# Optimization experiments

Hardware: AMD Instinct MI355X
Metric: run time of the kernel (lower is better)

Reference implementation:

```python
import jax, jax.numpy as jnp
import numpy as np

B, N, F_IN, H, HID = 2, 1024, 128, 4, 32  # batch, nodes, in_feat, heads, hidden per head


def setup_inputs() -> dict:
    key = jax.random.key(0)
    k1, k2, k3, k4 = jax.random.split(key, 4)
    node_feat = jax.random.normal(k1, (B, N, F_IN), dtype=jnp.float32)
    adj_mtx = jax.random.randint(k2, (B, N, N), 0, 2, dtype=jnp.int32)  # 0/1 adjacency
    # xavier_normal init for params
    W = jax.random.normal(k3, (F_IN, H * HID), dtype=jnp.float32) * np.sqrt(2.0 / (F_IN + H * HID))
    Wa = jax.random.normal(k4, (H, HID), dtype=jnp.float32) * np.sqrt(2.0 / (H + HID))
    return {"node_feat": node_feat, "adj_mtx": adj_mtx, "W": W, "Wa": Wa}


def reference(node_feat, adj_mtx, W, Wa):
    b, n, _ = node_feat.shape
    h, hid = Wa.shape
    # projected features: (B, H, N, hid)
    x = (node_feat @ W).reshape(b, n, h, hid).transpose(0, 2, 1, 3)
    # GATv2 additive scores: leaky_relu(x_i + x_j) . Wa  -> (B, H, N, N)
    s = jax.nn.leaky_relu(x[:, :, :, None, :] + x[:, :, None, :, :], negative_slope=0.2)
    e = jnp.einsum('bhijk,hk->bhij', s, Wa)
    # mask non-edges, softmax over neighbors j
    e = jnp.where(adj_mtx[:, None, :, :] > 0, e, -jnp.inf)
    att = jax.nn.softmax(e, axis=-1)
    # aggregate values: (B, H, N, hid)
    xp = jnp.einsum('bhij,bhjd->bhid', att, x)
    # concat heads -> (B, N, H*hid)
    return xp.transpose(0, 2, 1, 3).reshape(b, n, h * hid)
```

## Files before the change

kernel.cpp:

```cpp
#include <hip/hip_runtime.h>
#include <math.h>

#define BB 2
#define NN 1024
#define HH 4
#define F_IN 128
#define HID 32
#define TJ 64
#define NT (NN/TJ)
#define NC 2
#define CT (NT/NC)

#define LOG2E 1.44269504f

typedef unsigned long long u64;
typedef _Float16 f16;
typedef _Float16 f16x8 __attribute__((ext_vector_type(8)));
typedef _Float16 f16x4 __attribute__((ext_vector_type(4)));
typedef float f32x4 __attribute__((ext_vector_type(4)));

#define WS_X    0
#define WS_D6   1048576
#define WS_XT   1081344
#define WS_P    1605632
#define WS_LS   18382848

__global__ __launch_bounds__(128) void gat_proj_kernel(const float* __restrict__ feat,
        const float* __restrict__ W, const float* __restrict__ Wa,
        float* __restrict__ xout, f16* __restrict__ xt, float* __restrict__ d6) {
    const int RPB = 4;
    int blk = blockIdx.x;
    int b  = blk / (NN / RPB);
    int n0 = (blk % (NN / RPB)) * RPB;
    int t  = threadIdx.x;

    __shared__ float fs[RPB][F_IN];
#pragma unroll
    for (int e = 0; e < RPB; ++e) {
        int idx = e * 128 + t;
        int r = idx >> 7, f = idx & 127;
        fs[r][f] = feat[((size_t)(b*NN + n0 + r))*F_IN + f];
    }
    __syncthreads();

    float acc[RPB];
#pragma unroll
    for (int r = 0; r < RPB; ++r) acc[r] = 0.f;
    for (int f = 0; f < F_IN; ++f) {
        float w = W[f*(HH*HID) + t];
#pragma unroll
        for (int r = 0; r < RPB; ++r) acc[r] = fmaf(fs[r][f], w, acc[r]);
    }

    int h = t >> 5, k = t & 31;
    int bh = b*HH + h;
#pragma unroll
    for (int r = 0; r < RPB; ++r)
        xout[((size_t)bh*NN + n0 + r)*HID + k] = acc[r];
    {
        f16x4 hv;
#pragma unroll
        for (int r = 0; r < RPB; ++r) hv[r] = (f16)acc[r];
        *(f16x4*)(xt + ((size_t)bh*HID + k)*NN + n0) = hv;
    }
    float w_t = Wa[t];
#pragma unroll
    for (int r = 0; r < RPB; ++r) {
        float p = acc[r] * w_t;
#pragma unroll
        for (int off = 16; off >= 1; off >>= 1) p += __shfl_xor(p, off, 32);
        if (k == 0) d6[(size_t)bh*NN + n0 + r] = 0.6f * LOG2E * p;
    }
}

__device__ __forceinline__ float sload(float v) {
    return __uint_as_float(__builtin_amdgcn_readfirstlane(__float_as_uint(v)));
}

__global__ __launch_bounds__(256) void gat_score_kernel(const float* __restrict__ x,
                                                        const float* __restrict__ d6,
                                                        const int* __restrict__ adj,
                                                        const float* __restrict__ Wa,
                                                        f16* __restrict__ P,
                                                        float* __restrict__ lsp) {
    const int tid = threadIdx.x;
    const int w = __builtin_amdgcn_readfirstlane(tid >> 6);
    const int l = tid & 63;
    const int blk = blockIdx.x;
    const int bh = blk & 7;
    const int rest = blk >> 3;
    const int jc = rest & (NC - 1);
    const int i0 = (rest >> 1) << 3;
    const int h = bh & (HH - 1), b = bh >> 2;
    const int iA = i0 + 2*w, iB = iA + 1;

    const float* xbh = x  + (size_t)bh * NN * HID;
    const float* dbh = d6 + (size_t)bh * NN;
    const int* adjA = adj + ((size_t)b*NN + iA) * NN;
    const int* adjB = adj + ((size_t)b*NN + iB) * NN;

    float xiA[HID], xiB[HID], wa4[HID];
    {
        const float4* xAv = (const float4*)(xbh + (size_t)iA*HID);
        const float4* xBv = (const float4*)(xbh + (size_t)iB*HID);
        const float4* wav = (const float4*)(Wa + h*HID);
#pragma unroll
        for (int q = 0; q < 8; ++q) {
            float4 a = xAv[q], bq = xBv[q], wv = wav[q];
            xiA[4*q+0] = sload(a.x);  xiA[4*q+1] = sload(a.y);
            xiA[4*q+2] = sload(a.z);  xiA[4*q+3] = sload(a.w);
            xiB[4*q+0] = sload(bq.x); xiB[4*q+1] = sload(bq.y);
            xiB[4*q+2] = sload(bq.z); xiB[4*q+3] = sload(bq.w);
            wa4[4*q+0] = sload((0.4f*LOG2E)*wv.x); wa4[4*q+1] = sload((0.4f*LOG2E)*wv.y);
            wa4[4*q+2] = sload((0.4f*LOG2E)*wv.z); wa4[4*q+3] = sload((0.4f*LOG2E)*wv.w);
        }
    }
    float ciA = sload(dbh[iA]) - 8.0f;
    float ciB = sload(dbh[iB]) - 8.0f;

    __shared__ float xs[2][TJ][36];

    float lsA = 0.f, lsB = 0.f;
    f16* prA = P + ((size_t)bh << 20) + (size_t)iA * NN;
    f16* prB = P + ((size_t)bh << 20) + (size_t)iB * NN;

    const int r0 = tid >> 3,         q0 = (tid & 7) << 2;
    const int r1 = (tid + 256) >> 3, q1 = ((tid + 256) & 7) << 2;
    const float4* gsrc = (const float4*)xbh;
    const int t0 = jc * CT;
    float4 pre0 = gsrc[t0*512 + tid];
    float4 pre1 = gsrc[t0*512 + tid + 256];

    for (int tt = 0; tt < CT; ++tt) {
        const int tg = t0 + tt;
        const int bc = tt & 1;
        *(float4*)&xs[bc][r0][q0] = pre0;
        *(float4*)&xs[bc][r1][q1] = pre1;
        __syncthreads();
        if (tt + 1 < CT) {
            pre0 = gsrc[(tg + 1)*512 + tid];
            pre1 = gsrc[(tg + 1)*512 + tid + 256];
        }

        const int j = tg*TJ + l;
        u64 wA = __ballot(adjA[j] > 0);
        u64 wB = __ballot(adjB[j] > 0);
        float dj = dbh[j];

        float4 xj4[8];
#pragma unroll
        for (int q = 0; q < 8; ++q) xj4[q] = *(const float4*)&xs[bc][l][4*q];

        float sA0 = 0.f, sA1 = 0.f, sA2 = 0.f, sA3 = 0.f;
        float sB0 = 0.f, sB1 = 0.f, sB2 = 0.f, sB3 = 0.f;
#pragma unroll
        for (int q = 0; q < 8; ++q) {
            float4 xv = xj4[q];
            float v;
            v = xiA[4*q+0] + xv.x; sA0 = fmaf(wa4[4*q+0], fabsf(v), sA0);
            v = xiA[4*q+1] + xv.y; sA1 = fmaf(wa4[4*q+1], fabsf(v), sA1);
            v = xiA[4*q+2] + xv.z; sA2 = fmaf(wa4[4*q+2], fabsf(v), sA2);
            v = xiA[4*q+3] + xv.w; sA3 = fmaf(wa4[4*q+3], fabsf(v), sA3);
            v = xiB[4*q+0] + xv.x; sB0 = fmaf(wa4[4*q+0], fabsf(v), sB0);
            v = xiB[4*q+1] + xv.y; sB1 = fmaf(wa4[4*q+1], fabsf(v), sB1);
            v = xiB[4*q+2] + xv.z; sB2 = fmaf(wa4[4*q+2], fabsf(v), sB2);
            v = xiB[4*q+3] + xv.w; sB3 = fmaf(wa4[4*q+3], fabsf(v), sB3);
        }
        float eA = (ciA + dj) + ((sA0 + sA1) + (sA2 + sA3));
        float eB = (ciB + dj) + ((sB0 + sB1) + (sB2 + sB3));
        float peA = exp2f(eA), peB = exp2f(eB);
        float pA, pB;
        asm("v_cndmask_b32 %0, 0, %1, %2" : "=v"(pA) : "v"(peA), "s"(wA));
        asm("v_cndmask_b32 %0, 0, %1, %2" : "=v"(pB) : "v"(peB), "s"(wB));
        lsA += pA;
        lsB += pB;
        prA[j] = (f16)pA;
        prB[j] = (f16)pB;
    }

#pragma unroll
    for (int off = 32; off >= 1; off >>= 1) {
        lsA += __shfl_xor(lsA, off, 64);
        lsB += __shfl_xor(lsB, off, 64);
    }
    if (l == 0) {
        lsp[(size_t)jc*(8*NN) + bh*NN + iA] = lsA;
        lsp[(size_t)jc*(8*NN) + bh*NN + iB] = lsB;
    }
}

__global__ __launch_bounds__(64) void gat_agg_kernel(const f16* __restrict__ P,
                                                     const f16* __restrict__ xt,
                                                     const float* __restrict__ lsp,
                                                     float* __restrict__ out) {
    const int l = threadIdx.x;
    const int blk = blockIdx.x;
    const int bh = blk & 7;
    const int it = blk >> 3;
    const int i0 = it << 4;
    const int b = bh >> 2, h = bh & 3;

    const f16* Pb  = P  + ((size_t)bh << 20);
    const f16* xtb = xt + (size_t)bh * HID * NN;

    f32x4 acc0 = {0.f, 0.f, 0.f, 0.f};
    f32x4 acc1 = {0.f, 0.f, 0.f, 0.f};
    const int lrow = l & 15, lslot = (l >> 4) << 3;

#pragma unroll
    for (int jt = 0; jt < 32; ++jt) {
        const int joff = jt*32 + lslot;
        f16x8 af = *(const f16x8*)(Pb  + (size_t)(i0 + lrow)*NN + joff);
        f16x8 b0 = *(const f16x8*)(xtb + (size_t)lrow*NN + joff);
        f16x8 b1 = *(const f16x8*)(xtb + (size_t)(16 + lrow)*NN + joff);
        acc0 = __builtin_amdgcn_mfma_f32_16x16x32_f16(af, b0, acc0, 0, 0, 0);
        acc1 = __builtin_amdgcn_mfma_f32_16x16x32_f16(af, b1, acc1, 0, 0, 0);
    }

#pragma unroll
    for (int r = 0; r < 4; ++r) {
        int row = i0 + ((l >> 4) << 2) + r;
        float ls = lsp[bh*NN + row] + lsp[8*NN + bh*NN + row];
        float inv = 1.0f / ls;
        float* orow = out + ((size_t)(b*NN + row))*(HH*HID) + h*HID;
        orow[lrow]      = acc0[r] * inv;
        orow[16 + lrow] = acc1[r] * inv;
    }
}

extern "C" void kernel_launch(void* const* d_in, const int* in_sizes, int n_in,
                              void* d_out, int out_size, void* d_ws, size_t ws_size,
                              hipStream_t stream) {
    const float* node_feat = (const float*)d_in[0];
    const int*   adj_mtx   = (const int*)d_in[1];
    const float* W         = (const float*)d_in[2];
    const float* Wa        = (const float*)d_in[3];
    float* out = (float*)d_out;

    char* ws = (char*)d_ws;
    float* x_ws  = (float*)(ws + WS_X);
    float* d6_ws = (float*)(ws + WS_D6);
    f16*   xt_ws = (f16*)(ws + WS_XT);
    f16*   P_ws  = (f16*)(ws + WS_P);
    float* ls_ws = (float*)(ws + WS_LS);

    hipLaunchKernelGGL(gat_proj_kernel, dim3(BB*NN/4), dim3(128), 0, stream,
                       node_feat, W, Wa, x_ws, xt_ws, d6_ws);
    hipLaunchKernelGGL(gat_score_kernel, dim3(BB*HH*NN/8 * NC), dim3(256), 0, stream,
                       x_ws, d6_ws, adj_mtx, Wa, P_ws, ls_ws);
    hipLaunchKernelGGL(gat_agg_kernel, dim3(8 * 64), dim3(64), 0, stream,
                       P_ws, xt_ws, ls_ws, out);
}
```

Measured before the change: 42.33 us.

## Compute GATv2 scores in packed fp16 with fdot2, four rows per wave

The projection now stores x in fp16 instead of fp32. The score kernel computes |xi+xj| with packed half adds and sign masking, and accumulates against Wa using fdot2. Each wave now handles four query rows instead of two, and the LDS staging of xj tiles with its barriers is dropped in favour of direct global loads. This halves the bytes read for x and the ALU ops per score, at the cost of fp16 rounding in the attention logits and no LDS reuse of xj across waves.

```diff
diff --git a/kernel.cpp b/kernel.cpp
--- a/kernel.cpp
+++ b/kernel.cpp
@@ -7,27 +7,40 @@
 #define F_IN 128
 #define HID 32
 #define TJ 64
-#define NT (NN/TJ)
+#define NT 16
 #define NC 2
 #define CT (NT/NC)
 
 #define LOG2E 1.44269504f
 
 typedef unsigned long long u64;
+typedef unsigned int u32;
 typedef _Float16 f16;
+typedef _Float16 h2   __attribute__((ext_vector_type(2)));
+typedef _Float16 f16x4 __attribute__((ext_vector_type(4)));
 typedef _Float16 f16x8 __attribute__((ext_vector_type(8)));
-typedef _Float16 f16x4 __attribute__((ext_vector_type(4)));
 typedef float f32x4 __attribute__((ext_vector_type(4)));
 
-#define WS_X    0
-#define WS_D6   1048576
-#define WS_XT   1081344
-#define WS_P    1605632
-#define WS_LS   18382848
+#define WS_XH  0
+#define WS_D6  524288
+#define WS_XT  557056
+#define WS_P   1081344
+#define WS_LS  17858560
+
+#if __has_builtin(__builtin_amdgcn_fdot2)
+#define FDOT2(a, b, c) __builtin_amdgcn_fdot2((a), (b), (c), false)
+#else
+static __device__ __forceinline__ float FDOT2(h2 a, h2 b, float c) {
+    return fmaf((float)a[0], (float)b[0], fmaf((float)a[1], (float)b[1], c));
+}
+#endif
+
+template <typename D, typename S>
+static __device__ __forceinline__ D bcast(S s) { return __builtin_bit_cast(D, s); }
 
 __global__ __launch_bounds__(128) void gat_proj_kernel(const float* __restrict__ feat,
         const float* __restrict__ W, const float* __restrict__ Wa,
-        float* __restrict__ xout, f16* __restrict__ xt, float* __restrict__ d6) {
+        f16* __restrict__ xh, f16* __restrict__ xt, float* __restrict__ d6) {
     const int RPB = 4;
     int blk = blockIdx.x;
     int b  = blk / (NN / RPB);
@@ -56,7 +69,7 @@
     int bh = b*HH + h;
 #pragma unroll
     for (int r = 0; r < RPB; ++r)
-        xout[((size_t)bh*NN + n0 + r)*HID + k] = acc[r];
+        xh[((size_t)bh*NN + n0 + r)*HID + k] = (f16)acc[r];
     {
         f16x4 hv;
 #pragma unroll
@@ -73,11 +86,9 @@
     }
 }
 
-__device__ __forceinline__ float sload(float v) {
-    return __uint_as_float(__builtin_amdgcn_readfirstlane(__float_as_uint(v)));
-}
-
-__global__ __launch_bounds__(256) void gat_score_kernel(const float* __restrict__ x,
+__device__ __forceinline__ u32 srfl(u32 v) { return __builtin_amdgcn_readfirstlane(v); }
+
+__global__ __launch_bounds__(256) void gat_score_kernel(const f16* __restrict__ xh,
                                                         const float* __restrict__ d6,
                                                         const int* __restrict__ adj,
                                                         const float* __restrict__ Wa,
@@ -90,102 +101,101 @@
     const int bh = blk & 7;
     const int rest = blk >> 3;
     const int jc = rest & (NC - 1);
-    const int i0 = (rest >> 1) << 3;
-    const int h = bh & (HH - 1), b = bh >> 2;
-    const int iA = i0 + 2*w, iB = iA + 1;
-
-    const float* xbh = x  + (size_t)bh * NN * HID;
-    const float* dbh = d6 + (size_t)bh * NN;
-    const int* adjA = adj + ((size_t)b*NN + iA) * NN;
-    const int* adjB = adj + ((size_t)b*NN + iB) * NN;
-
-    float xiA[HID], xiB[HID], wa4[HID];
+    const int i0 = (rest >> 1) << 4;
+    const int h = bh & 3, b = bh >> 2;
+    const int ib = i0 + 4*w;
+
+    const u32* xhu = (const u32*)(xh + (size_t)bh*NN*HID);
+    const float* dbh = d6 + (size_t)bh*NN;
+
+    u32 wa2[16];
     {
-        const float4* xAv = (const float4*)(xbh + (size_t)iA*HID);
-        const float4* xBv = (const float4*)(xbh + (size_t)iB*HID);
-        const float4* wav = (const float4*)(Wa + h*HID);
-#pragma unroll
-        for (int q = 0; q < 8; ++q) {
-            float4 a = xAv[q], bq = xBv[q], wv = wav[q];
-            xiA[4*q+0] = sload(a.x);  xiA[4*q+1] = sload(a.y);
-            xiA[4*q+2] = sload(a.z);  xiA[4*q+3] = sload(a.w);
-            xiB[4*q+0] = sload(bq.x); xiB[4*q+1] = sload(bq.y);
-            xiB[4*q+2] = sload(bq.z); xiB[4*q+3] = sload(bq.w);
-            wa4[4*q+0] = sload((0.4f*LOG2E)*wv.x); wa4[4*q+1] = sload((0.4f*LOG2E)*wv.y);
-            wa4[4*q+2] = sload((0.4f*LOG2E)*wv.z); wa4[4*q+3] = sload((0.4f*LOG2E)*wv.w);
+        const float* wap = Wa + h*HID;
+#pragma unroll
+        for (int q = 0; q < 16; ++q) {
+            h2 hw;
+            hw[0] = (f16)((0.4f*LOG2E) * wap[2*q]);
+            hw[1] = (f16)((0.4f*LOG2E) * wap[2*q+1]);
+            wa2[q] = srfl(bcast<u32>(hw));
         }
     }
-    float ciA = sload(dbh[iA]) - 8.0f;
-    float ciB = sload(dbh[iB]) - 8.0f;
-
-    __shared__ float xs[2][TJ][36];
-
-    float lsA = 0.f, lsB = 0.f;
-    f16* prA = P + ((size_t)bh << 20) + (size_t)iA * NN;
-    f16* prB = P + ((size_t)bh << 20) + (size_t)iB * NN;
-
-    const int r0 = tid >> 3,         q0 = (tid & 7) << 2;
-    const int r1 = (tid + 256) >> 3, q1 = ((tid + 256) & 7) << 2;
-    const float4* gsrc = (const float4*)xbh;
-    const int t0 = jc * CT;
-    float4 pre0 = gsrc[t0*512 + tid];
-    float4 pre1 = gsrc[t0*512 + tid + 256];
+    u32 xi2[4][16];
+    float ci[4];
+#pragma unroll
+    for (int r = 0; r < 4; ++r) {
+        const u32* xr = xhu + (size_t)(ib + r)*16;
+#pragma unroll
+        for (int q = 0; q < 16; ++q) xi2[r][q] = srfl(xr[q]);
+        ci[r] = __uint_as_float(srfl(__float_as_uint(dbh[ib + r]))) - 8.0f;
+    }
+
+    const int* adj0 = adj + ((size_t)b*NN + ib + 0)*NN;
+    const int* adj1 = adj + ((size_t)b*NN + ib + 1)*NN;
+    const int* adj2 = adj + ((size_t)b*NN + ib + 2)*NN;
+    const int* adj3 = adj + ((size_t)b*NN + ib + 3)*NN;
+    f16* pr0 = P + ((size_t)bh << 20) + (size_t)(ib + 0)*NN;
+    f16* pr1 = P + ((size_t)bh << 20) + (size_t)(ib + 1)*NN;
+    f16* pr2 = P + ((size_t)bh << 20) + (size_t)(ib + 2)*NN;
+    f16* pr3 = P + ((size_t)bh << 20) + (size_t)(ib + 3)*NN;
+
+    float ls0 = 0.f, ls1 = 0.f, ls2 = 0.f, ls3 = 0.f;
 
     for (int tt = 0; tt < CT; ++tt) {
-        const int tg = t0 + tt;
-        const int bc = tt & 1;
-        *(float4*)&xs[bc][r0][q0] = pre0;
-        *(float4*)&xs[bc][r1][q1] = pre1;
-        __syncthreads();
-        if (tt + 1 < CT) {
-            pre0 = gsrc[(tg + 1)*512 + tid];
-            pre1 = gsrc[(tg + 1)*512 + tid + 256];
+        const int j = (jc*CT + tt)*TJ + l;
+        u64 m0 = __ballot(adj0[j] > 0);
+        u64 m1 = __ballot(adj1[j] > 0);
+        u64 m2 = __ballot(adj2[j] > 0);
+        u64 m3 = __ballot(adj3[j] > 0);
+        float dj = dbh[j];
+
+        const u32* xjp = xhu + (size_t)j*16;
+        uint4 xa = *(const uint4*)(xjp);
+        uint4 xb = *(const uint4*)(xjp + 4);
+        uint4 xc = *(const uint4*)(xjp + 8);
+        uint4 xd = *(const uint4*)(xjp + 12);
+        u32 xj[16] = {xa.x, xa.y, xa.z, xa.w, xb.x, xb.y, xb.z, xb.w,
+                      xc.x, xc.y, xc.z, xc.w, xd.x, xd.y, xd.z, xd.w};
+
+        float s0 = 0.f, s1 = 0.f, s2 = 0.f, s3 = 0.f;
+#pragma unroll
+        for (int q = 0; q < 16; ++q) {
+            h2 xjh = bcast<h2>(xj[q]);
+            h2 wq  = bcast<h2>(wa2[q]);
+            h2 v; u32 a;
+            v = bcast<h2>(xi2[0][q]) + xjh; a = bcast<u32>(v) & 0x7fff7fffu;
+            s0 = FDOT2(bcast<h2>(a), wq, s0);
+            v = bcast<h2>(xi2[1][q]) + xjh; a = bcast<u32>(v) & 0x7fff7fffu;
+            s1 = FDOT2(bcast<h2>(a), wq, s1);
+            v = bcast<h2>(xi2[2][q]) + xjh; a = bcast<u32>(v) & 0x7fff7fffu;
+            s2 = FDOT2(bcast<h2>(a), wq, s2);
+            v = bcast<h2>(xi2[3][q]) + xjh; a = bcast<u32>(v) & 0x7fff7fffu;
+            s3 = FDOT2(bcast<h2>(a), wq, s3);
         }
-
-        const int j = tg*TJ + l;
-        u64 wA = __ballot(adjA[j] > 0);
-        u64 wB = __ballot(adjB[j] > 0);
-        float dj = dbh[j];
-
-        float4 xj4[8];
-#pragma unroll
-        for (int q = 0; q < 8; ++q) xj4[q] = *(const float4*)&xs[bc][l][4*q];
-
-        float sA0 = 0.f, sA1 = 0.f, sA2 = 0.f, sA3 = 0.f;
-        float sB0 = 0.f, sB1 = 0.f, sB2 = 0.f, sB3 = 0.f;
-#pragma unroll
-        for (int q = 0; q < 8; ++q) {
-            float4 xv = xj4[q];
-            float v;
-            v = xiA[4*q+0] + xv.x; sA0 = fmaf(wa4[4*q+0], fabsf(v), sA0);
-            v = xiA[4*q+1] + xv.y; sA1 = fmaf(wa4[4*q+1], fabsf(v), sA1);
-            v = xiA[4*q+2] + xv.z; sA2 = fmaf(wa4[4*q+2], fabsf(v), sA2);
-            v = xiA[4*q+3] + xv.w; sA3 = fmaf(wa4[4*q+3], fabsf(v), sA3);
-            v = xiB[4*q+0] + xv.x; sB0 = fmaf(wa4[4*q+0], fabsf(v), sB0);
-            v = xiB[4*q+1] + xv.y; sB1 = fmaf(wa4[4*q+1], fabsf(v), sB1);
-            v = xiB[4*q+2] + xv.z; sB2 = fmaf(wa4[4*q+2], fabsf(v), sB2);
-            v = xiB[4*q+3] + xv.w; sB3 = fmaf(wa4[4*q+3], fabsf(v), sB3);
-        }
-        float eA = (ciA + dj) + ((sA0 + sA1) + (sA2 + sA3));
-        float eB = (ciB + dj) + ((sB0 + sB1) + (sB2 + sB3));
-        float peA = exp2f(eA), peB = exp2f(eB);
-        float pA, pB;
-        asm("v_cndmask_b32 %0, 0, %1, %2" : "=v"(pA) : "v"(peA), "s"(wA));
-        asm("v_cndmask_b32 %0, 0, %1, %2" : "=v"(pB) : "v"(peB), "s"(wB));
-        lsA += pA;
-        lsB += pB;
-        prA[j] = (f16)pA;
-        prB[j] = (f16)pB;
+        float p0 = exp2f(ci[0] + dj + s0);
+        float p1 = exp2f(ci[1] + dj + s1);
+        float p2 = exp2f(ci[2] + dj + s2);
+        float p3 = exp2f(ci[3] + dj + s3);
+        asm("v_cndmask_b32 %0, 0, %1, %2" : "=v"(p0) : "v"(p0), "s"(m0));
+        asm("v_cndmask_b32 %0, 0, %1, %2" : "=v"(p1) : "v"(p1), "s"(m1));
+        asm("v_cndmask_b32 %0, 0, %1, %2" : "=v"(p2) : "v"(p2), "s"(m2));
+        asm("v_cndmask_b32 %0, 0, %1, %2" : "=v"(p3) : "v"(p3), "s"(m3));
+        ls0 += p0; ls1 += p1; ls2 += p2; ls3 += p3;
+        pr0[j] = (f16)p0;
+        pr1[j] = (f16)p1;
+        pr2[j] = (f16)p2;
+        pr3[j] = (f16)p3;
     }
 
 #pragma unroll
     for (int off = 32; off >= 1; off >>= 1) {
-        lsA += __shfl_xor(lsA, off, 64);
-        lsB += __shfl_xor(lsB, off, 64);
+        ls0 += __shfl_xor(ls0, off, 64);
+        ls1 += __shfl_xor(ls1, off, 64);
+        ls2 += __shfl_xor(ls2, off, 64);
+        ls3 += __shfl_xor(ls3, off, 64);
     }
     if (l == 0) {
-        lsp[(size_t)jc*(8*NN) + bh*NN + iA] = lsA;
-        lsp[(size_t)jc*(8*NN) + bh*NN + iB] = lsB;
+        float* lp = lsp + (size_t)jc*(8*NN) + bh*NN + ib;
+        lp[0] = ls0; lp[1] = ls1; lp[2] = ls2; lp[3] = ls3;
     }
 }
 
@@ -238,16 +248,16 @@
     float* out = (float*)d_out;
 
     char* ws = (char*)d_ws;
-    float* x_ws  = (float*)(ws + WS_X);
+    f16*   xh_ws = (f16*)(ws + WS_XH);
     float* d6_ws = (float*)(ws + WS_D6);
     f16*   xt_ws = (f16*)(ws + WS_XT);
     f16*   P_ws  = (f16*)(ws + WS_P);
     float* ls_ws = (float*)(ws + WS_LS);
 
     hipLaunchKernelGGL(gat_proj_kernel, dim3(BB*NN/4), dim3(128), 0, stream,
-                       node_feat, W, Wa, x_ws, xt_ws, d6_ws);
-    hipLaunchKernelGGL(gat_score_kernel, dim3(BB*HH*NN/8 * NC), dim3(256), 0, stream,
-                       x_ws, d6_ws, adj_mtx, Wa, P_ws, ls_ws);
-    hipLaunchKernelGGL(gat_agg_kernel, dim3(8 * 64), dim3(64), 0, stream,
+                       node_feat, W, Wa, xh_ws, xt_ws, d6_ws);
+    hipLaunchKernelGGL(gat_score_kernel, dim3(8 * (NN/16) * NC), dim3(256), 0, stream,
+                       xh_ws, d6_ws, adj_mtx, Wa, P_ws, ls_ws);
+    hipLaunchKernelGGL(gat_agg_kernel, dim3(8 * (NN/16)), dim3(64), 0, stream,
                        P_ws, xt_ws, ls_ws, out);
 }
```

After: 39.81 us. -6.0%, faster.
